# Optimization experiments

Hardware: AMD Instinct MI355X
Metric: run time of the kernel (lower is better)

The kernel has to match this reference:

```python
import jax, jax.numpy as jnp
import numpy as np

B, N, T, D = 8, 512, 64, 128
H = 8
DK = D // H
KS = 3
CAUSAL_PAD = KS - 1          # query conv: pad both sides, crop tail
SYM_PAD = (KS - 1) // 2      # key conv: 'same' padding


def setup_inputs() -> dict:
    key0 = jax.random.key(0)
    ks = jax.random.split(key0, 12)
    s = 0.05  # weight scale to keep activations in a sane range
    inp = {
        "query": jax.random.normal(ks[0], (B, N, T, D), jnp.float32),
        "key": jax.random.normal(ks[1], (B, N, T, D), jnp.float32),
        "value": jax.random.normal(ks[2], (B, N, T, D), jnp.float32),
        # causal mask (batch, T, T): 1 where attention allowed
        "mask": jnp.broadcast_to(jnp.tril(jnp.ones((T, T), jnp.int32)), (B, T, T)),
        "Wq": jax.random.normal(ks[3], (D, D, 1, KS), jnp.float32) * s,
        "bq": jax.random.normal(ks[4], (D,), jnp.float32) * s,
        "Wk": jax.random.normal(ks[5], (D, D, 1, KS), jnp.float32) * s,
        "bk": jax.random.normal(ks[6], (D,), jnp.float32) * s,
        "W0": jax.random.normal(ks[7], (D, D), jnp.float32) * s,
        "b0": jax.random.normal(ks[8], (D,), jnp.float32) * s,
        "W1": jax.random.normal(ks[9], (D, D), jnp.float32) * s,
        "b1": jax.random.normal(ks[10], (D,), jnp.float32) * s,
        "query_multi_segment": 0,
        "key_multi_segment": 1,
    }
    return inp


def _temporal_conv(x, W, b, pad):
    # x: (B, N, T, D) -> NCHW (B, D, N, T); W: (O, I, 1, K) OIHW
    xt = jnp.transpose(x, (0, 3, 1, 2))
    y = jax.lax.conv_general_dilated(
        xt, W, window_strides=(1, 1),
        padding=[(0, 0), (pad, pad)],
        dimension_numbers=("NCHW", "OIHW", "NCHW"))
    return y + b[None, :, None, None]  # (B, D, N, T')


def _to_heads(y_bdnt, nbatches):
    # (B, D, N, T) -> view (B, H, DK, N, T) -> permute -> (B, N, H, T, DK)
    Bb, Dd, Nn, Tt = y_bdnt.shape
    y = y_bdnt.reshape(Bb, H, DK, Nn, Tt)
    return jnp.transpose(y, (0, 3, 1, 4, 2))


def reference(query, key, value, mask, Wq, bq, Wk, bk, W0, b0, W1, b1,
              query_multi_segment, key_multi_segment):
    del query_multi_segment, key_multi_segment  # static: (False, True) branch, h_length == T
    nbatches = query.shape[0]

    # causal conv for query: pad (k-1) both sides, crop last (k-1)
    q = _temporal_conv(query, Wq, bq, CAUSAL_PAD)[:, :, :, :-CAUSAL_PAD]
    q = _to_heads(q, nbatches)                       # (B, N, H, T, DK)
    # 'same' conv for key
    k = _to_heads(_temporal_conv(key, Wk, bk, SYM_PAD), nbatches)  # (B, N, H, T, DK)

    # value linear: x @ W0.T + b0, then split heads
    v = jnp.einsum("bntd,ed->bnte", value, W0) + b0
    v = jnp.transpose(v.reshape(nbatches, N, T, H, DK), (0, 1, 3, 2, 4))  # (B, N, H, T, DK)

    scores = jnp.einsum("bnhqd,bnhkd->bnhqk", q, k) / jnp.sqrt(jnp.float32(DK))
    m = mask[:, None, None, :, :]                    # (B, 1, 1, T, T)
    scores = jnp.where(m == 0, jnp.float32(-1e9), scores)
    p_attn = jax.nn.softmax(scores, axis=-1)         # dropout p=0.0 -> identity

    x = jnp.einsum("bnhqk,bnhkd->bnhqd", p_attn, v)  # (B, N, H, T, DK)
    x = jnp.transpose(x, (0, 1, 3, 2, 4)).reshape(nbatches, N, T, H * DK)
    return jnp.einsum("bntd,ed->bnte", x, W1) + b1
```

## Files before the change

kernel.cpp:

```cpp
#include <hip/hip_runtime.h>
#include <stdint.h>

constexpr int Tt = 64;
constexpr int Dd = 128;
constexpr int BN = 4096;

typedef short s16x8 __attribute__((ext_vector_type(8)));
typedef short s16x4 __attribute__((ext_vector_type(4)));
typedef float f32x4 __attribute__((ext_vector_type(4)));

__device__ __forceinline__ short f2bf(float f) {
  uint32_t u = __builtin_bit_cast(uint32_t, f);
  u += 0x7FFFu + ((u >> 16) & 1u);
  return (short)(u >> 16);
}

#define SQ_OFF   0
#define SK_OFF   16384
#define SV_OFF   32768
#define SP_OFF   49152
#define LDS_TOTAL 65536

__device__ __forceinline__ int swz256(int row, int colElem) {
  return (row << 8) + ((colElem << 1) ^ ((row & 7) << 4));
}
__device__ __forceinline__ int swz128(int row, int colElem) {
  return (row << 7) + ((colElem << 1) ^ ((row & 7) << 4));
}

__global__ void prep_weights(const float* __restrict__ Wq, const float* __restrict__ Wk,
                             const float* __restrict__ W0, const float* __restrict__ W1,
                             short* __restrict__ ws) {
  int i = blockIdx.x * 256 + threadIdx.x;
  if (i >= 131072) return;
  if (i < 49152) {
    int s = i >> 14, rem = i & 16383, o = rem >> 7, ii = rem & 127;
    ws[i] = f2bf(Wq[(o * 128 + ii) * 3 + s]);
  } else if (i < 98304) {
    int j = i - 49152;
    int s = j >> 14, rem = j & 16383, o = rem >> 7, ii = rem & 127;
    ws[i] = f2bf(Wk[(o * 128 + ii) * 3 + s]);
  } else if (i < 114688) {
    ws[i] = f2bf(W0[i - 98304]);
  } else {
    ws[i] = f2bf(W1[i - 114688]);
  }
}

template <int NT, int SHIFT>
__device__ __forceinline__ void conv_proj(const unsigned char* smem, int srcOff,
                                          const short* __restrict__ w,
                                          int lane, int cb, f32x4 acc[4]) {
#pragma unroll
  for (int rb = 0; rb < 4; ++rb) acc[rb] = (f32x4){0.f, 0.f, 0.f, 0.f};
  const int col = cb * 16 + (lane & 15);
  const int ke = 8 * (lane >> 4);
#pragma unroll
  for (int s = 0; s < NT; ++s) {
    s16x8 bfrag[4];
#pragma unroll
    for (int kk = 0; kk < 4; ++kk)
      bfrag[kk] = *(const s16x8*)(w + (s << 14) + (col << 7) + kk * 32 + ke);
#pragma unroll
    for (int kk = 0; kk < 4; ++kk) {
#pragma unroll
      for (int rb = 0; rb < 4; ++rb) {
        const int tr = rb * 16 + (lane & 15) + s + SHIFT;
        s16x8 af = (s16x8){0, 0, 0, 0, 0, 0, 0, 0};
        if (tr >= 0 && tr < Tt)
          af = *(const s16x8*)(smem + srcOff + swz256(tr, kk * 32 + ke));
        acc[rb] = __builtin_amdgcn_mfma_f32_16x16x32_bf16(af, bfrag[kk], acc[rb], 0, 0, 0);
      }
    }
  }
}

__device__ __forceinline__ void writeback_n(unsigned char* smem, int dstOff,
                                            const f32x4 acc[4], float bv, int lane, int cb) {
  const int col = cb * 16 + (lane & 15);
#pragma unroll
  for (int rb = 0; rb < 4; ++rb)
#pragma unroll
    for (int r = 0; r < 4; ++r) {
      const int row = rb * 16 + (lane >> 4) * 4 + r;
      *(short*)(smem + dstOff + swz256(row, col)) = f2bf(acc[rb][r] + bv);
    }
}

__device__ __forceinline__ void writeback_t(unsigned char* smem, int dstOff,
                                            const f32x4 acc[4], float bv, int lane, int cb) {
  const int col = cb * 16 + (lane & 15);
#pragma unroll
  for (int rb = 0; rb < 4; ++rb)
#pragma unroll
    for (int r = 0; r < 4; ++r) {
      const int row = rb * 16 + (lane >> 4) * 4 + r;
      *(short*)(smem + dstOff + swz128(col, row)) = f2bf(acc[rb][r] + bv);
    }
}

__launch_bounds__(512, 4)
__global__ void fused_attn(const float* __restrict__ query, const float* __restrict__ key,
                           const float* __restrict__ value, const short* __restrict__ wsb,
                           const float* __restrict__ bq, const float* __restrict__ bk,
                           const float* __restrict__ b0, const float* __restrict__ b1,
                           float* __restrict__ out) {
  __shared__ unsigned char smem[LDS_TOTAL];
  const int bn = blockIdx.x;
  const int tid = threadIdx.x;
  const int wave = tid >> 6;
  const int lane = tid & 63;
  const size_t base = (size_t)bn * (Tt * Dd);

  {
#pragma unroll
    for (int t3 = 0; t3 < 3; ++t3) {
      const float* sp = (t3 == 0) ? query : (t3 == 1) ? key : value;
      const float4* s4 = (const float4*)(sp + base);
      const int off = (t3 == 0) ? SQ_OFF : (t3 == 1) ? SK_OFF : SV_OFF;
      for (int i = tid; i < 2048; i += 512) {
        float4 v = s4[i];
        int row = i >> 5, col = (i & 31) << 2;
        s16x4 b = {f2bf(v.x), f2bf(v.y), f2bf(v.z), f2bf(v.w)};
        *(s16x4*)(smem + off + swz256(row, col)) = b;
      }
    }
  }
  __syncthreads();

  const int cb = wave;
  f32x4 acc[4];

  conv_proj<3, -2>(smem, SQ_OFF, wsb + 0, lane, cb, acc);
  __syncthreads();
  writeback_n(smem, SQ_OFF, acc, bq[cb * 16 + (lane & 15)], lane, cb);

  conv_proj<3, -1>(smem, SK_OFF, wsb + 49152, lane, cb, acc);
  __syncthreads();
  writeback_n(smem, SK_OFF, acc, bk[cb * 16 + (lane & 15)], lane, cb);

  conv_proj<1, 0>(smem, SV_OFF, wsb + 98304, lane, cb, acc);
  __syncthreads();
  writeback_t(smem, SV_OFF, acc, b0[cb * 16 + (lane & 15)], lane, cb);
  __syncthreads();

  {
    const int rb = wave & 3, hh = wave >> 2;
#pragma unroll
    for (int hi = 0; hi < 4; ++hi) {
      const int h = hh * 4 + hi;
      f32x4 sacc[4];
#pragma unroll
      for (int c = 0; c < 4; ++c) sacc[c] = (f32x4){0.f, 0.f, 0.f, 0.f};
      s16x8 af = (s16x8){0, 0, 0, 0, 0, 0, 0, 0};
      if (lane < 32)
        af = *(const s16x8*)(smem + SQ_OFF + swz256(rb * 16 + (lane & 15), h * 16 + 8 * (lane >> 4)));
#pragma unroll
      for (int c = 0; c < 4; ++c) {
        s16x8 bf = (s16x8){0, 0, 0, 0, 0, 0, 0, 0};
        if (lane < 32)
          bf = *(const s16x8*)(smem + SK_OFF + swz256(c * 16 + (lane & 15), h * 16 + 8 * (lane >> 4)));
        sacc[c] = __builtin_amdgcn_mfma_f32_16x16x32_bf16(af, bf, sacc[c], 0, 0, 0);
      }
      const int r0 = rb * 16 + (lane >> 4) * 4;
      float p[4][4], mx[4], sm[4];
#pragma unroll
      for (int r = 0; r < 4; ++r) mx[r] = -3.0e38f;
#pragma unroll
      for (int c = 0; c < 4; ++c) {
        const int col = c * 16 + (lane & 15);
#pragma unroll
        for (int r = 0; r < 4; ++r) {
          float sv = (col <= r0 + r) ? sacc[c][r] * 0.25f : -3.0e38f;
          p[c][r] = sv;
          mx[r] = fmaxf(mx[r], sv);
        }
      }
#pragma unroll
      for (int off = 1; off < 16; off <<= 1) {
#pragma unroll
        for (int r = 0; r < 4; ++r) mx[r] = fmaxf(mx[r], __shfl_xor(mx[r], off));
      }
#pragma unroll
      for (int r = 0; r < 4; ++r) sm[r] = 0.f;
#pragma unroll
      for (int c = 0; c < 4; ++c) {
#pragma unroll
        for (int r = 0; r < 4; ++r) {
          float e = __expf(p[c][r] - mx[r]);
          p[c][r] = e;
          sm[r] += e;
        }
      }
#pragma unroll
      for (int off = 1; off < 16; off <<= 1) {
#pragma unroll
        for (int r = 0; r < 4; ++r) sm[r] += __shfl_xor(sm[r], off);
      }
      float inv[4];
#pragma unroll
      for (int r = 0; r < 4; ++r) inv[r] = 1.0f / sm[r];
      unsigned char* sp = smem + SP_OFF + wave * 2048;
#pragma unroll
      for (int c = 0; c < 4; ++c) {
#pragma unroll
        for (int r = 0; r < 4; ++r)
          *(short*)(sp + swz128((lane >> 4) * 4 + r, c * 16 + (lane & 15))) = f2bf(p[c][r] * inv[r]);
      }
      asm volatile("s_waitcnt lgkmcnt(0)" ::: "memory");
      f32x4 xacc = (f32x4){0.f, 0.f, 0.f, 0.f};
#pragma unroll
      for (int kc = 0; kc < 2; ++kc) {
        s16x8 pf = *(const s16x8*)(sp + swz128(lane & 15, kc * 32 + 8 * (lane >> 4)));
        s16x8 vf = *(const s16x8*)(smem + SV_OFF + swz128(h * 16 + (lane & 15), kc * 32 + 8 * (lane >> 4)));
        xacc = __builtin_amdgcn_mfma_f32_16x16x32_bf16(pf, vf, xacc, 0, 0, 0);
      }
#pragma unroll
      for (int r = 0; r < 4; ++r)
        *(short*)(smem + SQ_OFF + swz256(rb * 16 + (lane >> 4) * 4 + r, h * 16 + (lane & 15))) = f2bf(xacc[r]);
      asm volatile("s_waitcnt lgkmcnt(0)" ::: "memory");
    }
  }
  __syncthreads();

  {
    const short* w1 = wsb + 114688;
    const int col = cb * 16 + (lane & 15);
    const int ke = 8 * (lane >> 4);
    s16x8 bfrag[4];
#pragma unroll
    for (int kk = 0; kk < 4; ++kk)
      bfrag[kk] = *(const s16x8*)(w1 + (col << 7) + kk * 32 + ke);
    f32x4 oacc[4];
#pragma unroll
    for (int rb = 0; rb < 4; ++rb) oacc[rb] = (f32x4){0.f, 0.f, 0.f, 0.f};
#pragma unroll
    for (int kk = 0; kk < 4; ++kk) {
#pragma unroll
      for (int rb = 0; rb < 4; ++rb) {
        s16x8 af = *(const s16x8*)(smem + SQ_OFF + swz256(rb * 16 + (lane & 15), kk * 32 + ke));
        oacc[rb] = __builtin_amdgcn_mfma_f32_16x16x32_bf16(af, bfrag[kk], oacc[rb], 0, 0, 0);
      }
    }
    const float bv = b1[col];
#pragma unroll
    for (int rb = 0; rb < 4; ++rb)
#pragma unroll
      for (int r = 0; r < 4; ++r) {
        const int row = rb * 16 + (lane >> 4) * 4 + r;
        out[base + (size_t)row * Dd + col] = oacc[rb][r] + bv;
      }
  }
}

extern "C" void kernel_launch(void* const* d_in, const int* in_sizes, int n_in,
                              void* d_out, int out_size, void* d_ws, size_t ws_size,
                              hipStream_t stream) {
  (void)in_sizes; (void)n_in; (void)out_size; (void)ws_size;
  const float* query = (const float*)d_in[0];
  const float* key   = (const float*)d_in[1];
  const float* value = (const float*)d_in[2];
  const float* Wq = (const float*)d_in[4];
  const float* bq = (const float*)d_in[5];
  const float* Wk = (const float*)d_in[6];
  const float* bk = (const float*)d_in[7];
  const float* W0 = (const float*)d_in[8];
  const float* b0 = (const float*)d_in[9];
  const float* W1 = (const float*)d_in[10];
  const float* b1 = (const float*)d_in[11];
  float* out = (float*)d_out;
  short* wsb = (short*)d_ws;

  hipLaunchKernelGGL(prep_weights, dim3(512), dim3(256), 0, stream, Wq, Wk, W0, W1, wsb);
  hipLaunchKernelGGL(fused_attn, dim3(BN), dim3(512), 0, stream,
                     query, key, value, wsb, bq, bk, b0, b1, out);
}
```

Before: 249.5 us.

## Merge Q/K/V projections into one pass with zero-padded halo rows

Computes the Q, K and V projections in a single phase, keeping all accumulators live, and removes the intermediate barriers between projections. Padded zero rows are added to the Q/K LDS buffers so the conv loads need no bounds checks. Masked lanes in the score MFMA read a zero row instead of branching. The softmax normalisation is deferred until after P·V, the P buffer gets an extra swizzle bit, and the W1 fragments are prefetched early. The trade-off is higher register pressure from three accumulator sets and a larger LDS footprint, which may lower occupancy.

```diff
diff --git a/kernel.cpp b/kernel.cpp
--- a/kernel.cpp
+++ b/kernel.cpp
@@ -1,4 +1,5 @@
 #include <hip/hip_runtime.h>
+#include <hip/hip_bf16.h>
 #include <stdint.h>
 
 constexpr int Tt = 64;
@@ -10,22 +11,23 @@
 typedef float f32x4 __attribute__((ext_vector_type(4)));
 
 __device__ __forceinline__ short f2bf(float f) {
-  uint32_t u = __builtin_bit_cast(uint32_t, f);
-  u += 0x7FFFu + ((u >> 16) & 1u);
-  return (short)(u >> 16);
+  return (short)__bfloat16_as_ushort(__float2bfloat16(f));
 }
 
 #define SQ_OFF   0
-#define SK_OFF   16384
-#define SV_OFF   32768
-#define SP_OFF   49152
-#define LDS_TOTAL 65536
+#define SK_OFF   17408
+#define SV_OFF   34816
+#define SP_OFF   51200
+#define LDS_TOTAL 67584
 
 __device__ __forceinline__ int swz256(int row, int colElem) {
   return (row << 8) + ((colElem << 1) ^ ((row & 7) << 4));
 }
 __device__ __forceinline__ int swz128(int row, int colElem) {
   return (row << 7) + ((colElem << 1) ^ ((row & 7) << 4));
+}
+__device__ __forceinline__ int swzP(int row, int colElem) {
+  return (row << 7) + (((colElem << 1) ^ ((row & 7) << 4)) ^ ((row & 8) << 2));
 }
 
 __global__ void prep_weights(const float* __restrict__ Wq, const float* __restrict__ Wk,
@@ -47,58 +49,6 @@
   }
 }
 
-template <int NT, int SHIFT>
-__device__ __forceinline__ void conv_proj(const unsigned char* smem, int srcOff,
-                                          const short* __restrict__ w,
-                                          int lane, int cb, f32x4 acc[4]) {
-#pragma unroll
-  for (int rb = 0; rb < 4; ++rb) acc[rb] = (f32x4){0.f, 0.f, 0.f, 0.f};
-  const int col = cb * 16 + (lane & 15);
-  const int ke = 8 * (lane >> 4);
-#pragma unroll
-  for (int s = 0; s < NT; ++s) {
-    s16x8 bfrag[4];
-#pragma unroll
-    for (int kk = 0; kk < 4; ++kk)
-      bfrag[kk] = *(const s16x8*)(w + (s << 14) + (col << 7) + kk * 32 + ke);
-#pragma unroll
-    for (int kk = 0; kk < 4; ++kk) {
-#pragma unroll
-      for (int rb = 0; rb < 4; ++rb) {
-        const int tr = rb * 16 + (lane & 15) + s + SHIFT;
-        s16x8 af = (s16x8){0, 0, 0, 0, 0, 0, 0, 0};
-        if (tr >= 0 && tr < Tt)
-          af = *(const s16x8*)(smem + srcOff + swz256(tr, kk * 32 + ke));
-        acc[rb] = __builtin_amdgcn_mfma_f32_16x16x32_bf16(af, bfrag[kk], acc[rb], 0, 0, 0);
-      }
-    }
-  }
-}
-
-__device__ __forceinline__ void writeback_n(unsigned char* smem, int dstOff,
-                                            const f32x4 acc[4], float bv, int lane, int cb) {
-  const int col = cb * 16 + (lane & 15);
-#pragma unroll
-  for (int rb = 0; rb < 4; ++rb)
-#pragma unroll
-    for (int r = 0; r < 4; ++r) {
-      const int row = rb * 16 + (lane >> 4) * 4 + r;
-      *(short*)(smem + dstOff + swz256(row, col)) = f2bf(acc[rb][r] + bv);
-    }
-}
-
-__device__ __forceinline__ void writeback_t(unsigned char* smem, int dstOff,
-                                            const f32x4 acc[4], float bv, int lane, int cb) {
-  const int col = cb * 16 + (lane & 15);
-#pragma unroll
-  for (int rb = 0; rb < 4; ++rb)
-#pragma unroll
-    for (int r = 0; r < 4; ++r) {
-      const int row = rb * 16 + (lane >> 4) * 4 + r;
-      *(short*)(smem + dstOff + swz128(col, row)) = f2bf(acc[rb][r] + bv);
-    }
-}
-
 __launch_bounds__(512, 4)
 __global__ void fused_attn(const float* __restrict__ query, const float* __restrict__ key,
                            const float* __restrict__ value, const short* __restrict__ wsb,
@@ -112,54 +62,119 @@
   const int lane = tid & 63;
   const size_t base = (size_t)bn * (Tt * Dd);
 
+  const int cb = wave;
+  const int col = cb * 16 + (lane & 15);
+  const int ke = 8 * (lane >> 4);
+  const int arow = lane & 15;
+
+  if (tid < 128) {
+    int bufOff = (tid >= 64) ? SK_OFF : SQ_OFF;
+    int ri = (tid >> 4) & 3;
+    int row = (ri < 2) ? ri : 64 + ri;
+    s16x8 z = {};
+    *(s16x8*)(smem + bufOff + swz256(row, (tid & 15) * 8)) = z;
+  }
   {
 #pragma unroll
     for (int t3 = 0; t3 < 3; ++t3) {
       const float* sp = (t3 == 0) ? query : (t3 == 1) ? key : value;
       const float4* s4 = (const float4*)(sp + base);
       const int off = (t3 == 0) ? SQ_OFF : (t3 == 1) ? SK_OFF : SV_OFF;
+      const int rshift = (t3 == 2) ? 0 : 2;
       for (int i = tid; i < 2048; i += 512) {
         float4 v = s4[i];
-        int row = i >> 5, col = (i & 31) << 2;
+        int row = (i >> 5) + rshift, c4 = (i & 31) << 2;
         s16x4 b = {f2bf(v.x), f2bf(v.y), f2bf(v.z), f2bf(v.w)};
-        *(s16x4*)(smem + off + swz256(row, col)) = b;
-      }
-    }
-  }
-  __syncthreads();
-
-  const int cb = wave;
-  f32x4 acc[4];
-
-  conv_proj<3, -2>(smem, SQ_OFF, wsb + 0, lane, cb, acc);
-  __syncthreads();
-  writeback_n(smem, SQ_OFF, acc, bq[cb * 16 + (lane & 15)], lane, cb);
-
-  conv_proj<3, -1>(smem, SK_OFF, wsb + 49152, lane, cb, acc);
-  __syncthreads();
-  writeback_n(smem, SK_OFF, acc, bk[cb * 16 + (lane & 15)], lane, cb);
-
-  conv_proj<1, 0>(smem, SV_OFF, wsb + 98304, lane, cb, acc);
-  __syncthreads();
-  writeback_t(smem, SV_OFF, acc, b0[cb * 16 + (lane & 15)], lane, cb);
+        *(s16x4*)(smem + off + swz256(row, c4)) = b;
+      }
+    }
+  }
+  __syncthreads();
+
+  f32x4 aq[4], ak[4], av[4];
+#pragma unroll
+  for (int rb = 0; rb < 4; ++rb) {
+    aq[rb] = (f32x4){0.f, 0.f, 0.f, 0.f};
+    ak[rb] = (f32x4){0.f, 0.f, 0.f, 0.f};
+    av[rb] = (f32x4){0.f, 0.f, 0.f, 0.f};
+  }
+  const short* wq = wsb;
+  const short* wk = wsb + 49152;
+  const short* wv = wsb + 98304;
+  const short* w1 = wsb + 114688;
+
+#pragma unroll
+  for (int s = 0; s < 3; ++s) {
+    s16x8 bq8[4], bk8[4];
+#pragma unroll
+    for (int kk = 0; kk < 4; ++kk) {
+      bq8[kk] = *(const s16x8*)(wq + (s << 14) + (col << 7) + kk * 32 + ke);
+      bk8[kk] = *(const s16x8*)(wk + (s << 14) + (col << 7) + kk * 32 + ke);
+    }
+#pragma unroll
+    for (int kk = 0; kk < 4; ++kk) {
+#pragma unroll
+      for (int rb = 0; rb < 4; ++rb) {
+        s16x8 afq = *(const s16x8*)(smem + SQ_OFF + swz256(rb * 16 + arow + s, kk * 32 + ke));
+        aq[rb] = __builtin_amdgcn_mfma_f32_16x16x32_bf16(afq, bq8[kk], aq[rb], 0, 0, 0);
+        s16x8 afk = *(const s16x8*)(smem + SK_OFF + swz256(rb * 16 + arow + s + 1, kk * 32 + ke));
+        ak[rb] = __builtin_amdgcn_mfma_f32_16x16x32_bf16(afk, bk8[kk], ak[rb], 0, 0, 0);
+      }
+    }
+  }
+  {
+    s16x8 bv8[4];
+#pragma unroll
+    for (int kk = 0; kk < 4; ++kk)
+      bv8[kk] = *(const s16x8*)(wv + (col << 7) + kk * 32 + ke);
+#pragma unroll
+    for (int kk = 0; kk < 4; ++kk) {
+#pragma unroll
+      for (int rb = 0; rb < 4; ++rb) {
+        s16x8 afv = *(const s16x8*)(smem + SV_OFF + swz256(rb * 16 + arow, kk * 32 + ke));
+        av[rb] = __builtin_amdgcn_mfma_f32_16x16x32_bf16(afv, bv8[kk], av[rb], 0, 0, 0);
+      }
+    }
+  }
+  __syncthreads();
+
+  {
+    const float bqv = bq[col], bkv = bk[col], b0v = b0[col];
+#pragma unroll
+    for (int rb = 0; rb < 4; ++rb) {
+#pragma unroll
+      for (int r = 0; r < 4; ++r) {
+        const int row = rb * 16 + (lane >> 4) * 4 + r;
+        *(short*)(smem + SQ_OFF + swz256(row, col)) = f2bf(aq[rb][r] + bqv);
+        *(short*)(smem + SK_OFF + swz256(row, col)) = f2bf(ak[rb][r] + bkv);
+        *(short*)(smem + SV_OFF + swz128(col, row)) = f2bf(av[rb][r] + b0v);
+      }
+    }
+  }
+  s16x8 w1f[4];
+#pragma unroll
+  for (int kk = 0; kk < 4; ++kk)
+    w1f[kk] = *(const s16x8*)(w1 + (col << 7) + kk * 32 + ke);
   __syncthreads();
 
   {
     const int rb = wave & 3, hh = wave >> 2;
+    const int sel = lane >> 5;
+    const int aRow = sel ? 66 : (rb * 16 + arow);
+    int bRow[4];
+#pragma unroll
+    for (int c = 0; c < 4; ++c) bRow[c] = sel ? 66 : (c * 16 + arow);
+    unsigned char* sp = smem + SP_OFF + wave * 2048;
 #pragma unroll
     for (int hi = 0; hi < 4; ++hi) {
       const int h = hh * 4 + hi;
       f32x4 sacc[4];
 #pragma unroll
       for (int c = 0; c < 4; ++c) sacc[c] = (f32x4){0.f, 0.f, 0.f, 0.f};
-      s16x8 af = (s16x8){0, 0, 0, 0, 0, 0, 0, 0};
-      if (lane < 32)
-        af = *(const s16x8*)(smem + SQ_OFF + swz256(rb * 16 + (lane & 15), h * 16 + 8 * (lane >> 4)));
-#pragma unroll
-      for (int c = 0; c < 4; ++c) {
-        s16x8 bf = (s16x8){0, 0, 0, 0, 0, 0, 0, 0};
-        if (lane < 32)
-          bf = *(const s16x8*)(smem + SK_OFF + swz256(c * 16 + (lane & 15), h * 16 + 8 * (lane >> 4)));
+      s16x8 af = *(const s16x8*)(smem + SQ_OFF + swz256(aRow, h * 16 + ke));
+#pragma unroll
+      for (int c = 0; c < 4; ++c) {
+        s16x8 bf = *(const s16x8*)(smem + SK_OFF + swz256(bRow[c], h * 16 + ke));
         sacc[c] = __builtin_amdgcn_mfma_f32_16x16x32_bf16(af, bf, sacc[c], 0, 0, 0);
       }
       const int r0 = rb * 16 + (lane >> 4) * 4;
@@ -168,10 +183,10 @@
       for (int r = 0; r < 4; ++r) mx[r] = -3.0e38f;
 #pragma unroll
       for (int c = 0; c < 4; ++c) {
-        const int col = c * 16 + (lane & 15);
+        const int scol = c * 16 + (lane & 15);
 #pragma unroll
         for (int r = 0; r < 4; ++r) {
-          float sv = (col <= r0 + r) ? sacc[c][r] * 0.25f : -3.0e38f;
+          float sv = (scol <= r0 + r) ? sacc[c][r] * 0.25f : -3.0e38f;
           p[c][r] = sv;
           mx[r] = fmaxf(mx[r], sv);
         }
@@ -200,37 +215,30 @@
       float inv[4];
 #pragma unroll
       for (int r = 0; r < 4; ++r) inv[r] = 1.0f / sm[r];
-      unsigned char* sp = smem + SP_OFF + wave * 2048;
 #pragma unroll
       for (int c = 0; c < 4; ++c) {
 #pragma unroll
         for (int r = 0; r < 4; ++r)
-          *(short*)(sp + swz128((lane >> 4) * 4 + r, c * 16 + (lane & 15))) = f2bf(p[c][r] * inv[r]);
+          *(short*)(sp + swzP((lane >> 4) * 4 + r, c * 16 + (lane & 15))) = f2bf(p[c][r]);
       }
       asm volatile("s_waitcnt lgkmcnt(0)" ::: "memory");
       f32x4 xacc = (f32x4){0.f, 0.f, 0.f, 0.f};
 #pragma unroll
       for (int kc = 0; kc < 2; ++kc) {
-        s16x8 pf = *(const s16x8*)(sp + swz128(lane & 15, kc * 32 + 8 * (lane >> 4)));
-        s16x8 vf = *(const s16x8*)(smem + SV_OFF + swz128(h * 16 + (lane & 15), kc * 32 + 8 * (lane >> 4)));
+        s16x8 pf = *(const s16x8*)(sp + swzP(arow, kc * 32 + ke));
+        s16x8 vf = *(const s16x8*)(smem + SV_OFF + swz128(h * 16 + arow, kc * 32 + ke));
         xacc = __builtin_amdgcn_mfma_f32_16x16x32_bf16(pf, vf, xacc, 0, 0, 0);
       }
 #pragma unroll
       for (int r = 0; r < 4; ++r)
-        *(short*)(smem + SQ_OFF + swz256(rb * 16 + (lane >> 4) * 4 + r, h * 16 + (lane & 15))) = f2bf(xacc[r]);
+        *(short*)(smem + SQ_OFF + swz256(rb * 16 + (lane >> 4) * 4 + r, h * 16 + (lane & 15))) =
+            f2bf(xacc[r] * inv[r]);
       asm volatile("s_waitcnt lgkmcnt(0)" ::: "memory");
     }
   }
   __syncthreads();
 
   {
-    const short* w1 = wsb + 114688;
-    const int col = cb * 16 + (lane & 15);
-    const int ke = 8 * (lane >> 4);
-    s16x8 bfrag[4];
-#pragma unroll
-    for (int kk = 0; kk < 4; ++kk)
-      bfrag[kk] = *(const s16x8*)(w1 + (col << 7) + kk * 32 + ke);
     f32x4 oacc[4];
 #pragma unroll
     for (int rb = 0; rb < 4; ++rb) oacc[rb] = (f32x4){0.f, 0.f, 0.f, 0.f};
@@ -238,8 +246,8 @@
     for (int kk = 0; kk < 4; ++kk) {
 #pragma unroll
       for (int rb = 0; rb < 4; ++rb) {
-        s16x8 af = *(const s16x8*)(smem + SQ_OFF + swz256(rb * 16 + (lane & 15), kk * 32 + ke));
-        oacc[rb] = __builtin_amdgcn_mfma_f32_16x16x32_bf16(af, bfrag[kk], oacc[rb], 0, 0, 0);
+        s16x8 af = *(const s16x8*)(smem + SQ_OFF + swz256(rb * 16 + arow, kk * 32 + ke));
+        oacc[rb] = __builtin_amdgcn_mfma_f32_16x16x32_bf16(af, w1f[kk], oacc[rb], 0, 0, 0);
       }
     }
     const float bv = b1[col];
```

New measurement: 242.0 us. 1.03x faster.
